# Optimization experiments

Measured on AMD Instinct MI355X. Metric: run time of the kernel, lower is better.

Reference implementation:

```python
import jax, jax.numpy as jnp
import numpy as np

V, N, H, A_DIM, F_OUT = 3, 8192, 128, 64, 128


def setup_inputs() -> dict:
    key = jax.random.key(0)
    ks = jax.random.split(key, 13)
    s = 0.02
    w = lambda k, shape: jax.random.normal(k, shape, jnp.float32) * s
    adj = jax.random.randint(ks[0], (V, N, N), 0, 2, dtype=jnp.int32)
    return {
        "adjacency_matrices_list": adj,
        "W1": w(ks[1], (V, N, H)), "b1": w(ks[2], (V, H)),
        "W2": w(ks[3], (V, H, H)), "b2": w(ks[4], (V, H)),
        "Wa1": w(ks[5], (H, A_DIM)), "ba1": w(ks[6], (A_DIM,)),
        "Wa2": w(ks[7], (A_DIM, 1)), "ba2": w(ks[8], (1,)),
        "Wf1": w(ks[9], (H * V, 2 * H)), "bf1": w(ks[10], (2 * H,)),
        "Wf2": w(ks[11], (2 * H, F_OUT)), "bf2": w(ks[12], (F_OUT,)),
    }


def _norm_adj(adj_int):
    # PyG GCNConv gcn_norm on binary edges: add remaining self-loops, then D^-1/2 (A+I) D^-1/2
    a = (adj_int != 0).astype(jnp.float32)            # (V,N,N) binary
    eye = jnp.eye(adj_int.shape[-1], dtype=jnp.float32)
    ah = a * (1.0 - eye) + eye                        # force diagonal to exactly 1
    dinv = jax.lax.rsqrt(ah.sum(-1))                  # deg >= 1, safe
    return ah * dinv[..., :, None] * dinv[..., None, :]


def _forward(adj, W1, b1, W2, b2, Wa1, ba1, Wa2, ba2, Wf1, bf1, Wf2, bf2):
    A = _norm_adj(adj)                                # (V,N,N)
    # initial features X = eye(N), so A @ (X @ W1) == A @ W1
    h = jax.nn.relu(jnp.einsum('vnm,vmh->vnh', A, W1) + b1[:, None, :])
    h = jnp.einsum('vnh,vhk->vnk', h, W2)
    h = jax.nn.relu(jnp.einsum('vnm,vmk->vnk', A, h) + b2[:, None, :])  # (V,N,H) view embeddings
    # attention fusion
    summ = h.mean(axis=1)                             # (V,H) view summaries
    scores = (jnp.tanh(summ @ Wa1 + ba1) @ Wa2 + ba2)[:, 0]
    attn = jax.nn.softmax(scores, axis=0)             # (V,)
    weighted = h * attn[:, None, None]
    fusion_in = jnp.transpose(weighted, (1, 0, 2)).reshape(h.shape[1], -1)  # (N, V*H)
    fused = jax.nn.relu(fusion_in @ Wf1 + bf1) @ Wf2 + bf2                  # (N, F_OUT)
    return fused, attn, h


def reference(adjacency_matrices_list, W1, b1, W2, b2, Wa1, ba1, Wa2, ba2, Wf1, bf1, Wf2, bf2):
    return _forward(adjacency_matrices_list, W1, b1, W2, b2, Wa1, ba1, Wa2, ba2, Wf1, bf1, Wf2, bf2)
```

## Files before the change

kernel.cpp:

```cpp
#include <hip/hip_runtime.h>
#include <hip/hip_bf16.h>

#define VV 3
#define NN 8192
#define HH 128
#define ADIM 64
#define FOUT 128
#define KSPLIT 4

typedef short bf16x8 __attribute__((ext_vector_type(8)));
typedef float f32x4 __attribute__((ext_vector_type(4)));

__device__ __forceinline__ float bf2f(ushort u) {
    union { unsigned int i; float f; } x; x.i = ((unsigned int)u) << 16; return x.f;
}
__device__ __forceinline__ ushort f2bf(float f) {
    union { float f; unsigned int i; } x; x.f = f;
    unsigned int r = (x.i + 0x7FFFu + ((x.i >> 16) & 1u)) >> 16;
    return (ushort)r;
}
__device__ __forceinline__ void async_cp16(const ushort* g, ushort* l) {
    __builtin_amdgcn_global_load_lds(
        (const __attribute__((address_space(1))) void*)g,
        (__attribute__((address_space(3))) void*)l, 16, 0, 0);
}

__global__ void zero_k(float* p, int n) {
    int i = blockIdx.x * blockDim.x + threadIdx.x;
    if (i < n) p[i] = 0.0f;
}

__global__ __launch_bounds__(256) void pack_k(const int* __restrict__ adj,
                                              ushort* __restrict__ apack,
                                              float* __restrict__ dinv) {
    const int w = threadIdx.x >> 6, lane = threadIdx.x & 63;
    const long rowg = (long)blockIdx.x * 4 + w;
    const int i = (int)(rowg & (NN - 1));
    const int* row = adj + rowg * NN;
    ushort* prow = apack + rowg * NN;
    int cnt = 0;
    #pragma unroll 4
    for (int it = 0; it < 32; it++) {
        const int c0 = it * 256 + lane * 4;
        const int4 v = *(const int4*)(row + c0);
        ushort4 o;
        o.x = (v.x != 0 || c0 + 0 == i) ? (ushort)0x3F80 : (ushort)0;
        o.y = (v.y != 0 || c0 + 1 == i) ? (ushort)0x3F80 : (ushort)0;
        o.z = (v.z != 0 || c0 + 2 == i) ? (ushort)0x3F80 : (ushort)0;
        o.w = (v.w != 0 || c0 + 3 == i) ? (ushort)0x3F80 : (ushort)0;
        cnt += (o.x != 0) + (o.y != 0) + (o.z != 0) + (o.w != 0);
        *(ushort4*)(prow + c0) = o;
    }
    for (int off = 32; off; off >>= 1) cnt += __shfl_down(cnt, off);
    if (lane == 0) dinv[rowg] = rsqrtf((float)cnt);
}

template<int INF32>
__global__ void transpose_scale_k(const void* __restrict__ in_, ushort* __restrict__ out,
                                  int R, int C, const float* __restrict__ scale, int scale_z) {
    __shared__ ushort tile[32][33];
    const long zo = (long)blockIdx.z * R * C;
    const int c0 = blockIdx.x * 32, r0 = blockIdx.y * 32;
    const int t = threadIdx.x;
    #pragma unroll
    for (int p = 0; p < 4; p++) {
        int e = p * 256 + t; int row = e >> 5, col = e & 31;
        long idx = zo + (long)(r0 + row) * C + c0 + col;
        float x = INF32 ? ((const float*)in_)[idx] : bf2f(((const ushort*)in_)[idx]);
        if (scale) x *= scale[(long)blockIdx.z * scale_z + r0 + row];
        tile[row][col] = f2bf(x);
    }
    __syncthreads();
    #pragma unroll
    for (int p = 0; p < 4; p++) {
        int e = p * 256 + t; int row = e >> 5, col = e & 31;
        out[zo + (long)(c0 + row) * R + r0 + col] = tile[col][row];
    }
}

__global__ __launch_bounds__(256) void gemm_adj_k(
    const ushort* __restrict__ Apack,
    const ushort* __restrict__ Bt,
    float* __restrict__ Cpart)
{
    __shared__ __align__(16) ushort As[128 * 64];
    __shared__ __align__(16) ushort Bs[128 * 64];
    const int tid = threadIdx.x, lane = tid & 63, w = tid >> 6;
    const int wr = w >> 1, wc = w & 1;
    const int ks = blockIdx.x, mt = blockIdx.y, z = blockIdx.z;
    const int m0 = mt * 128;
    const int kbeg = ks * (NN / KSPLIT);
    const ushort* Av = Apack + (long)z * NN * NN;
    const ushort* Bv = Bt + (long)z * 128 * NN;
    f32x4 acc[4][4] = {};

    int srow[4], slcb[4];
    #pragma unroll
    for (int p = 0; p < 4; p++) {
        int slot = (w * 4 + p) * 64 + lane;
        srow[p] = slot >> 3;
        slcb[p] = (slot & 7) ^ (srow[p] & 7);
    }

    for (int k0 = kbeg; k0 < kbeg + NN / KSPLIT; k0 += 64) {
        #pragma unroll
        for (int p = 0; p < 4; p++) {
            const int slot = (w * 4 + p) * 64 + lane;
            async_cp16(Av + (long)(m0 + srow[p]) * NN + k0 + slcb[p] * 8, As + slot * 8);
            async_cp16(Bv + (long)srow[p] * NN + k0 + slcb[p] * 8, Bs + slot * 8);
        }
        __syncthreads();
        #pragma unroll
        for (int s = 0; s < 2; s++) {
            bf16x8 af[4], bb[4];
            const int ca = s * 4 + (lane >> 4);
            #pragma unroll
            for (int mi = 0; mi < 4; mi++) {
                int r = wr * 64 + mi * 16 + (lane & 15);
                af[mi] = *(const bf16x8*)&As[r * 64 + ((ca ^ (r & 7)) * 8)];
            }
            #pragma unroll
            for (int ni = 0; ni < 4; ni++) {
                int r = wc * 64 + ni * 16 + (lane & 15);
                bb[ni] = *(const bf16x8*)&Bs[r * 64 + ((ca ^ (r & 7)) * 8)];
            }
            #pragma unroll
            for (int mi = 0; mi < 4; mi++)
                #pragma unroll
                for (int ni = 0; ni < 4; ni++)
                    acc[mi][ni] = __builtin_amdgcn_mfma_f32_16x16x32_bf16(af[mi], bb[ni], acc[mi][ni], 0, 0, 0);
        }
        __syncthreads();
    }

    float* C = Cpart + ((long)ks * VV + z) * ((long)NN * HH);
    #pragma unroll
    for (int mi = 0; mi < 4; mi++) {
        int rbase = m0 + wr * 64 + mi * 16 + ((lane >> 4) << 2);
        #pragma unroll
        for (int ni = 0; ni < 4; ni++) {
            int col = wc * 64 + ni * 16 + (lane & 15);
            #pragma unroll
            for (int r = 0; r < 4; r++)
                C[(long)(rbase + r) * HH + col] = acc[mi][ni][r];
        }
    }
}

template<int WRITE_F32>
__global__ __launch_bounds__(256) void reduce_k(const float* __restrict__ P,
                                                const float* __restrict__ dinv,
                                                const float* __restrict__ bias,
                                                ushort* __restrict__ hout,
                                                float* __restrict__ fout) {
    const long e = ((long)blockIdx.x * 256 + threadIdx.x) * 4;
    const int v = (int)(e >> 20);
    const int n = (int)((e >> 7) & (NN - 1));
    const int col = (int)(e & 127);
    const long S = (long)VV * NN * HH;
    const float4 s0 = *(const float4*)(P + e);
    const float4 s1 = *(const float4*)(P + S + e);
    const float4 s2 = *(const float4*)(P + 2 * S + e);
    const float4 s3 = *(const float4*)(P + 3 * S + e);
    const float d = dinv[v * NN + n];
    const float r0 = fmaxf((s0.x + s1.x + s2.x + s3.x) * d + bias[v * HH + col + 0], 0.f);
    const float r1 = fmaxf((s0.y + s1.y + s2.y + s3.y) * d + bias[v * HH + col + 1], 0.f);
    const float r2 = fmaxf((s0.z + s1.z + s2.z + s3.z) * d + bias[v * HH + col + 2], 0.f);
    const float r3 = fmaxf((s0.w + s1.w + s2.w + s3.w) * d + bias[v * HH + col + 3], 0.f);
    ushort4 o; o.x = f2bf(r0); o.y = f2bf(r1); o.z = f2bf(r2); o.w = f2bf(r3);
    *(ushort4*)(hout + e) = o;
    if (WRITE_F32) { float4 f; f.x = r0; f.y = r1; f.z = r2; f.w = r3; *(float4*)(fout + e) = f; }
}

template<int AMODE, int EPI, int OUTF32>
__global__ __launch_bounds__(256) void gemm_k(
    const void* __restrict__ Aany, long a_zs, int lda,
    const ushort* __restrict__ Bt, long b_zs, int ldb,
    void* __restrict__ Cc, long c_zs, int ldc,
    int Ktot,
    const float* __restrict__ dinv, int dinv_zs,
    const float* __restrict__ bias, int bias_zs,
    const float* __restrict__ attnp)
{
    __shared__ __align__(16) ushort As[128][40];
    __shared__ __align__(16) ushort Bs[128][40];
    const int tid = threadIdx.x;
    const int bx = blockIdx.x, by = blockIdx.y, z = blockIdx.z;
    const int m0 = by * 128, n0 = bx * 128;
    const int lane = tid & 63, w = tid >> 6, wr = w >> 1, wc = w & 1;
    f32x4 acc[4][4] = {};
    float att0 = 0.f, att1 = 0.f, att2 = 0.f;
    if (AMODE == 2) { att0 = attnp[0]; att1 = attnp[1]; att2 = attnp[2]; }
    const ushort* Ab = (const ushort*)Aany + (long)z * (AMODE == 1 ? a_zs : 0);
    const ushort* Btz = Bt + (long)z * b_zs;

    for (int k0 = 0; k0 < Ktot; k0 += 32) {
        if (AMODE == 1) {
            #pragma unroll
            for (int p = 0; p < 2; p++) {
                int c = p * 256 + tid;
                int row = c >> 2, q = c & 3;
                *(int4*)&As[row][q * 8] = *(const int4*)(Ab + (long)(m0 + row) * lda + k0 + q * 8);
            }
        } else {
            #pragma unroll
            for (int p = 0; p < 2; p++) {
                int c = p * 256 + tid;
                int row = c >> 2, q = c & 3;
                int kk = k0 + q * 8;
                int v = kk >> 7, ko = kk & 127;
                int4 raw = *(const int4*)((const ushort*)Aany + (long)v * a_zs + (long)(m0 + row) * HH + ko);
                float sc = (v == 0) ? att0 : (v == 1 ? att1 : att2);
                __align__(16) ushort us[8];
                *(int4*)us = raw;
                #pragma unroll
                for (int e = 0; e < 8; e++) us[e] = f2bf(bf2f(us[e]) * sc);
                *(int4*)&As[row][q * 8] = *(int4*)us;
            }
        }
        #pragma unroll
        for (int p = 0; p < 2; p++) {
            int c = p * 256 + tid;
            int n = c >> 2, q = c & 3;
            *(int4*)&Bs[n][q * 8] = *(const int4*)(Btz + (long)(n0 + n) * ldb + k0 + q * 8);
        }
        __syncthreads();
        bf16x8 af[4], bfr[4];
        #pragma unroll
        for (int mi = 0; mi < 4; mi++)
            af[mi] = *(const bf16x8*)&As[wr * 64 + mi * 16 + (lane & 15)][(lane >> 4) * 8];
        #pragma unroll
        for (int ni = 0; ni < 4; ni++)
            bfr[ni] = *(const bf16x8*)&Bs[wc * 64 + ni * 16 + (lane & 15)][(lane >> 4) * 8];
        #pragma unroll
        for (int mi = 0; mi < 4; mi++)
            #pragma unroll
            for (int ni = 0; ni < 4; ni++)
                acc[mi][ni] = __builtin_amdgcn_mfma_f32_16x16x32_bf16(af[mi], bfr[ni], acc[mi][ni], 0, 0, 0);
        __syncthreads();
    }

    #pragma unroll
    for (int mi = 0; mi < 4; mi++) {
        int rbase = m0 + wr * 64 + mi * 16 + ((lane >> 4) << 2);
        #pragma unroll
        for (int ni = 0; ni < 4; ni++) {
            int col = n0 + wc * 64 + ni * 16 + (lane & 15);
            #pragma unroll
            for (int r = 0; r < 4; r++) {
                int grow = rbase + r;
                float vv = acc[mi][ni][r];
                if (EPI == 1) vv *= dinv[(long)z * dinv_zs + grow];
                if (EPI == 2 || EPI == 3) vv += bias[col];
                if (EPI == 2) vv = fmaxf(vv, 0.0f);
                if (OUTF32) ((float*)Cc + (long)z * c_zs)[(long)grow * ldc + col] = vv;
                else        ((ushort*)Cc + (long)z * c_zs)[(long)grow * ldc + col] = f2bf(vv);
            }
        }
    }
}

__global__ __launch_bounds__(256) void colsum_k(const ushort* __restrict__ h2,
                                                float* __restrict__ summ) {
    const int rowbase = blockIdx.x * 64;
    const int z = rowbase >> 13;
    const int col = threadIdx.x & 127, half = threadIdx.x >> 7;
    float s = 0.0f;
    for (int r = half; r < 64; r += 2) s += bf2f(h2[(long)(rowbase + r) * HH + col]);
    atomicAdd(&summ[z * HH + col], s);
}

__global__ __launch_bounds__(256) void attn_k(const float* __restrict__ summ,
                                              const float* __restrict__ Wa1,
                                              const float* __restrict__ ba1,
                                              const float* __restrict__ Wa2,
                                              const float* __restrict__ ba2,
                                              float* __restrict__ attnws,
                                              float* __restrict__ out_attn) {
    __shared__ float sc[VV];
    const int tid = threadIdx.x;
    if (tid < VV * 64) {
        const int v = tid >> 6, a = tid & 63;
        float s = ba1[a];
        const float invN = 1.0f / (float)NN;
        #pragma unroll 4
        for (int h = 0; h < HH; h++) s += summ[v * HH + h] * invN * Wa1[h * ADIM + a];
        float p = tanhf(s) * Wa2[a];
        for (int off = 32; off; off >>= 1) p += __shfl_down(p, off);
        if (a == 0) sc[v] = p + ba2[0];
    }
    __syncthreads();
    if (tid == 0) {
        float m = fmaxf(sc[0], fmaxf(sc[1], sc[2]));
        float e0 = expf(sc[0] - m), e1 = expf(sc[1] - m), e2 = expf(sc[2] - m);
        float inv = 1.0f / (e0 + e1 + e2);
        attnws[0] = e0 * inv; attnws[1] = e1 * inv; attnws[2] = e2 * inv;
        out_attn[0] = e0 * inv; out_attn[1] = e1 * inv; out_attn[2] = e2 * inv;
    }
}

extern "C" void kernel_launch(void* const* d_in, const int* in_sizes, int n_in,
                              void* d_out, int out_size, void* d_ws, size_t ws_size,
                              hipStream_t stream) {
    const int*   adj = (const int*)d_in[0];
    const float* W1  = (const float*)d_in[1];
    const float* b1  = (const float*)d_in[2];
    const float* W2  = (const float*)d_in[3];
    const float* b2  = (const float*)d_in[4];
    const float* Wa1 = (const float*)d_in[5];
    const float* ba1 = (const float*)d_in[6];
    const float* Wa2 = (const float*)d_in[7];
    const float* ba2 = (const float*)d_in[8];
    const float* Wf1 = (const float*)d_in[9];
    const float* bf1 = (const float*)d_in[10];
    const float* Wf2 = (const float*)d_in[11];
    const float* bf2v = (const float*)d_in[12];

    float* out = (float*)d_out;
    float* out_fused = out;
    float* out_attn  = out + (long)NN * FOUT;
    float* out_h     = out + (long)NN * FOUT + VV;

    char* wsb = (char*)d_ws;
    const long SZ_DINV  = (long)VV * NN * 4;
    const long SZ_APACK = (long)VV * NN * NN * 2;
    const long SZ_W1T   = (long)VV * HH * NN * 2;
    const long SZ_W2T   = (long)VV * HH * HH * 2;
    const long SZ_WF1T  = 256L * 384 * 2;
    const long SZ_WF2T  = 128L * 256 * 2;
    const long SZ_VNH   = (long)VV * NN * HH * 2;
    const long SZ_PART  = (long)KSPLIT * VV * NN * HH * 4;
    const long SZ_G     = (long)NN * 256 * 2;
    long off = 0;
    float*  dinv  = (float*)(wsb + off);  off += SZ_DINV;
    ushort* apack = (ushort*)(wsb + off); off += SZ_APACK;
    ushort* w1t   = (ushort*)(wsb + off); off += SZ_W1T;
    ushort* w2t   = (ushort*)(wsb + off); off += SZ_W2T;
    ushort* wf1t  = (ushort*)(wsb + off); off += SZ_WF1T;
    ushort* wf2t  = (ushort*)(wsb + off); off += SZ_WF2T;
    ushort* h1    = (ushort*)(wsb + off); off += SZ_VNH;
    ushort* tbuf  = (ushort*)(wsb + off); off += SZ_VNH;
    ushort* tT    = (ushort*)(wsb + off); off += SZ_VNH;
    ushort* h2    = (ushort*)(wsb + off); off += SZ_VNH;
    float*  cpart = (float*)(wsb + off);  off += SZ_PART;
    ushort* G     = (ushort*)(wsb + off); off += SZ_G;
    float*  summ  = (float*)(wsb + off);  off += 1536;
    float*  attnw = (float*)(wsb + off);  off += 16;

    const long VNH = (long)NN * HH;

    zero_k<<<1, 512, 0, stream>>>(summ, 388);
    pack_k<<<(VV * NN) / 4, 256, 0, stream>>>(adj, apack, dinv);
    transpose_scale_k<1><<<dim3(4, 256, VV), 256, 0, stream>>>(W1, w1t, NN, HH, dinv, NN);
    transpose_scale_k<1><<<dim3(4, 4, VV), 256, 0, stream>>>(W2, w2t, HH, HH, nullptr, 0);
    transpose_scale_k<1><<<dim3(8, 12, 1), 256, 0, stream>>>(Wf1, wf1t, 384, 256, nullptr, 0);
    transpose_scale_k<1><<<dim3(4, 8, 1), 256, 0, stream>>>(Wf2, wf2t, 256, 128, nullptr, 0);
    gemm_adj_k<<<dim3(KSPLIT, 64, VV), 256, 0, stream>>>(apack, w1t, cpart);
    reduce_k<0><<<3072, 256, 0, stream>>>(cpart, dinv, b1, h1, nullptr);
    gemm_k<1, 1, 0><<<dim3(1, 64, VV), 256, 0, stream>>>(h1, VNH, HH, w2t, (long)HH * HH, HH,
                                                         tbuf, VNH, HH, HH, dinv, NN, nullptr, 0, nullptr);
    transpose_scale_k<0><<<dim3(4, 256, VV), 256, 0, stream>>>(tbuf, tT, NN, HH, nullptr, 0);
    gemm_adj_k<<<dim3(KSPLIT, 64, VV), 256, 0, stream>>>(apack, tT, cpart);
    reduce_k<1><<<3072, 256, 0, stream>>>(cpart, dinv, b2, h2, out_h);
    colsum_k<<<(VV * NN) / 64, 256, 0, stream>>>(h2, summ);
    attn_k<<<1, 256, 0, stream>>>(summ, Wa1, ba1, Wa2, ba2, attnw, out_attn);
    gemm_k<2, 2, 0><<<dim3(2, 64, 1), 256, 0, stream>>>(h2, VNH, HH, wf1t, 0, 384,
                                                        G, 0, 256, 384, nullptr, 0, bf1, 0, attnw);
    gemm_k<1, 3, 1><<<dim3(1, 64, 1), 256, 0, stream>>>(G, 0, 256, wf2t, 0, 256,
                                                        out_fused, 0, FOUT, 256, nullptr, 0, bf2v, 0, nullptr);
}
```

Measured before the change: 1.453 ms.

## Bit-pack normalized adjacency and expand bits to bf16 inside the GEMM

The pack kernel now stores the binary adjacency (with self-loops) as 1-bit masks, laid out tile-contiguously per GEMM block, instead of as a full bf16 matrix. It accumulates degrees with atomics, and a separate kernel computes the rsqrt normalizers. The adjacency GEMM loads 1 KB of bits per k-step and expands them into bf16 MFMA operands in registers. This cuts the packed-adjacency write and its two rereads by 16x. The cost is extra ALU work for bit expansion, plus atomics and an extra small kernel.

```diff
diff --git a/kernel.cpp b/kernel.cpp
--- a/kernel.cpp
+++ b/kernel.cpp
@@ -10,6 +10,7 @@
 
 typedef short bf16x8 __attribute__((ext_vector_type(8)));
 typedef float f32x4 __attribute__((ext_vector_type(4)));
+typedef unsigned char uchar;
 
 __device__ __forceinline__ float bf2f(ushort u) {
     union { unsigned int i; float f; } x; x.i = ((unsigned int)u) << 16; return x.f;
@@ -19,7 +20,7 @@
     unsigned int r = (x.i + 0x7FFFu + ((x.i >> 16) & 1u)) >> 16;
     return (ushort)r;
 }
-__device__ __forceinline__ void async_cp16(const ushort* g, ushort* l) {
+__device__ __forceinline__ void async_cp16(const void* g, void* l) {
     __builtin_amdgcn_global_load_lds(
         (const __attribute__((address_space(1))) void*)g,
         (__attribute__((address_space(3))) void*)l, 16, 0, 0);
@@ -31,28 +32,43 @@
 }
 
 __global__ __launch_bounds__(256) void pack_k(const int* __restrict__ adj,
-                                              ushort* __restrict__ apack,
-                                              float* __restrict__ dinv) {
-    const int w = threadIdx.x >> 6, lane = threadIdx.x & 63;
-    const long rowg = (long)blockIdx.x * 4 + w;
-    const int i = (int)(rowg & (NN - 1));
-    const int* row = adj + rowg * NN;
-    ushort* prow = apack + rowg * NN;
+                                              uchar* __restrict__ abits,
+                                              int* __restrict__ deg) {
+    __shared__ uint lw[32 * 256];
+    const int t = threadIdx.x;
+    const int r = t >> 1, half = t & 1;
+    const int ks = blockIdx.x, mt = blockIdx.y, z = blockIdx.z;
+    const int m0 = mt * 128;
+    const int n = m0 + r;
+    const long rowoff = ((long)z * NN + n) * NN;
     int cnt = 0;
-    #pragma unroll 4
-    for (int it = 0; it < 32; it++) {
-        const int c0 = it * 256 + lane * 4;
-        const int4 v = *(const int4*)(row + c0);
-        ushort4 o;
-        o.x = (v.x != 0 || c0 + 0 == i) ? (ushort)0x3F80 : (ushort)0;
-        o.y = (v.y != 0 || c0 + 1 == i) ? (ushort)0x3F80 : (ushort)0;
-        o.z = (v.z != 0 || c0 + 2 == i) ? (ushort)0x3F80 : (ushort)0;
-        o.w = (v.w != 0 || c0 + 3 == i) ? (ushort)0x3F80 : (ushort)0;
-        cnt += (o.x != 0) + (o.y != 0) + (o.z != 0) + (o.w != 0);
-        *(ushort4*)(prow + c0) = o;
-    }
-    for (int off = 32; off; off >>= 1) cnt += __shfl_down(cnt, off);
-    if (lane == 0) dinv[rowg] = rsqrtf((float)cnt);
+    for (int kc = 0; kc < 32; kc++) {
+        const int colbase = ks * (NN / KSPLIT) + kc * 64 + half * 32;
+        uint wbits = 0;
+        #pragma unroll
+        for (int i = 0; i < 8; i++) {
+            const int c0 = colbase + i * 4;
+            const int4 v = *(const int4*)(adj + rowoff + c0);
+            uint b0 = (v.x != 0 || c0 + 0 == n) ? 1u : 0u;
+            uint b1 = (v.y != 0 || c0 + 1 == n) ? 1u : 0u;
+            uint b2 = (v.z != 0 || c0 + 2 == n) ? 1u : 0u;
+            uint b3 = (v.w != 0 || c0 + 3 == n) ? 1u : 0u;
+            wbits |= (b0 | (b1 << 1) | (b2 << 2) | (b3 << 3)) << (i * 4);
+        }
+        cnt += __popc(wbits);
+        lw[kc * 256 + r * 2 + half] = wbits;
+    }
+    atomicAdd(&deg[z * NN + n], cnt);
+    __syncthreads();
+    const uint4* src = (const uint4*)lw;
+    uint4* dst = (uint4*)(abits + ((((long)z * 64 + mt) * 128 + ks * 32) << 10));
+    #pragma unroll
+    for (int it = 0; it < 8; it++) dst[it * 256 + t] = src[it * 256 + t];
+}
+
+__global__ void dinv_k(const int* __restrict__ deg, float* __restrict__ dinv) {
+    int i = blockIdx.x * blockDim.x + threadIdx.x;
+    if (i < VV * NN) dinv[i] = rsqrtf((float)deg[i]);
 }
 
 template<int INF32>
@@ -79,18 +95,18 @@
 }
 
 __global__ __launch_bounds__(256) void gemm_adj_k(
-    const ushort* __restrict__ Apack,
+    const uchar* __restrict__ abits,
     const ushort* __restrict__ Bt,
     float* __restrict__ Cpart)
 {
-    __shared__ __align__(16) ushort As[128 * 64];
+    __shared__ __align__(16) uchar As[1024];
     __shared__ __align__(16) ushort Bs[128 * 64];
     const int tid = threadIdx.x, lane = tid & 63, w = tid >> 6;
     const int wr = w >> 1, wc = w & 1;
     const int ks = blockIdx.x, mt = blockIdx.y, z = blockIdx.z;
     const int m0 = mt * 128;
     const int kbeg = ks * (NN / KSPLIT);
-    const ushort* Av = Apack + (long)z * NN * NN;
+    const uchar* Atile = abits + (((long)z * 64 + mt) * 128 << 10);
     const ushort* Bv = Bt + (long)z * 128 * NN;
     f32x4 acc[4][4] = {};
 
@@ -103,22 +119,30 @@
     }
 
     for (int k0 = kbeg; k0 < kbeg + NN / KSPLIT; k0 += 64) {
+        if (w == 0)
+            async_cp16(Atile + ((long)(k0 >> 6) << 10) + lane * 16, As + lane * 16);
         #pragma unroll
         for (int p = 0; p < 4; p++) {
             const int slot = (w * 4 + p) * 64 + lane;
-            async_cp16(Av + (long)(m0 + srow[p]) * NN + k0 + slcb[p] * 8, As + slot * 8);
             async_cp16(Bv + (long)srow[p] * NN + k0 + slcb[p] * 8, Bs + slot * 8);
         }
         __syncthreads();
+        const int q = lane >> 4;
         #pragma unroll
         for (int s = 0; s < 2; s++) {
             bf16x8 af[4], bb[4];
-            const int ca = s * 4 + (lane >> 4);
             #pragma unroll
             for (int mi = 0; mi < 4; mi++) {
-                int r = wr * 64 + mi * 16 + (lane & 15);
-                af[mi] = *(const bf16x8*)&As[r * 64 + ((ca ^ (r & 7)) * 8)];
-            }
+                const int r = wr * 64 + mi * 16 + (lane & 15);
+                const uint b = As[r * 8 + s * 4 + q];
+                union { uint4 u; bf16x8 v; } cvt;
+                cvt.u.x = ((b     ) & 1u) * 0x00003F80u | ((b >> 1) & 1u) * 0x3F800000u;
+                cvt.u.y = ((b >> 2) & 1u) * 0x00003F80u | ((b >> 3) & 1u) * 0x3F800000u;
+                cvt.u.z = ((b >> 4) & 1u) * 0x00003F80u | ((b >> 5) & 1u) * 0x3F800000u;
+                cvt.u.w = ((b >> 6) & 1u) * 0x00003F80u | ((b >> 7) & 1u) * 0x3F800000u;
+                af[mi] = cvt.v;
+            }
+            const int ca = s * 4 + q;
             #pragma unroll
             for (int ni = 0; ni < 4; ni++) {
                 int r = wc * 64 + ni * 16 + (lane & 15);
@@ -323,7 +347,7 @@
 
     char* wsb = (char*)d_ws;
     const long SZ_DINV  = (long)VV * NN * 4;
-    const long SZ_APACK = (long)VV * NN * NN * 2;
+    const long SZ_ABITS = (long)VV * 64 * 128 * 1024;
     const long SZ_W1T   = (long)VV * HH * NN * 2;
     const long SZ_W2T   = (long)VV * HH * HH * 2;
     const long SZ_WF1T  = 256L * 384 * 2;
@@ -333,7 +357,7 @@
     const long SZ_G     = (long)NN * 256 * 2;
     long off = 0;
     float*  dinv  = (float*)(wsb + off);  off += SZ_DINV;
-    ushort* apack = (ushort*)(wsb + off); off += SZ_APACK;
+    uchar*  abits = (uchar*)(wsb + off);  off += SZ_ABITS;
     ushort* w1t   = (ushort*)(wsb + off); off += SZ_W1T;
     ushort* w2t   = (ushort*)(wsb + off); off += SZ_W2T;
     ushort* wf1t  = (ushort*)(wsb + off); off += SZ_WF1T;
@@ -344,23 +368,25 @@
     ushort* h2    = (ushort*)(wsb + off); off += SZ_VNH;
     float*  cpart = (float*)(wsb + off);  off += SZ_PART;
     ushort* G     = (ushort*)(wsb + off); off += SZ_G;
-    float*  summ  = (float*)(wsb + off);  off += 1536;
-    float*  attnw = (float*)(wsb + off);  off += 16;
+    float*  summ  = (float*)(wsb + off);  off += 1600;
+    float*  attnw = summ + 384;
+    int*    deg   = (int*)(wsb + off);    off += (long)VV * NN * 4;
 
     const long VNH = (long)NN * HH;
 
-    zero_k<<<1, 512, 0, stream>>>(summ, 388);
-    pack_k<<<(VV * NN) / 4, 256, 0, stream>>>(adj, apack, dinv);
+    zero_k<<<98, 256, 0, stream>>>(summ, 400 + VV * NN);
+    pack_k<<<dim3(KSPLIT, 64, VV), 256, 0, stream>>>(adj, abits, deg);
+    dinv_k<<<96, 256, 0, stream>>>(deg, dinv);
     transpose_scale_k<1><<<dim3(4, 256, VV), 256, 0, stream>>>(W1, w1t, NN, HH, dinv, NN);
     transpose_scale_k<1><<<dim3(4, 4, VV), 256, 0, stream>>>(W2, w2t, HH, HH, nullptr, 0);
     transpose_scale_k<1><<<dim3(8, 12, 1), 256, 0, stream>>>(Wf1, wf1t, 384, 256, nullptr, 0);
     transpose_scale_k<1><<<dim3(4, 8, 1), 256, 0, stream>>>(Wf2, wf2t, 256, 128, nullptr, 0);
-    gemm_adj_k<<<dim3(KSPLIT, 64, VV), 256, 0, stream>>>(apack, w1t, cpart);
+    gemm_adj_k<<<dim3(KSPLIT, 64, VV), 256, 0, stream>>>(abits, w1t, cpart);
     reduce_k<0><<<3072, 256, 0, stream>>>(cpart, dinv, b1, h1, nullptr);
     gemm_k<1, 1, 0><<<dim3(1, 64, VV), 256, 0, stream>>>(h1, VNH, HH, w2t, (long)HH * HH, HH,
                                                          tbuf, VNH, HH, HH, dinv, NN, nullptr, 0, nullptr);
     transpose_scale_k<0><<<dim3(4, 256, VV), 256, 0, stream>>>(tbuf, tT, NN, HH, nullptr, 0);
-    gemm_adj_k<<<dim3(KSPLIT, 64, VV), 256, 0, stream>>>(apack, tT, cpart);
+    gemm_adj_k<<<dim3(KSPLIT, 64, VV), 256, 0, stream>>>(abits, tT, cpart);
     reduce_k<1><<<3072, 256, 0, stream>>>(cpart, dinv, b2, h2, out_h);
     colsum_k<<<(VV * NN) / 64, 256, 0, stream>>>(h2, summ);
     attn_k<<<1, 256, 0, stream>>>(summ, Wa1, ba1, Wa2, ba2, attnw, out_attn);
```

After: 1.500 ms. +3.3%, slower.
